# Performance work log

Measured on AMD Instinct MI355X. Metric: run time of the kernel, lower is better.

The kernel has to match this reference:

```python
import jax, jax.numpy as jnp
import numpy as np

WIRES = 4
DIM = 16  # 2**WIRES
EPS = 1e-5


def _rot_matrix(phi, theta, omega):
    # PennyLane Rot = RZ(omega) RY(theta) RZ(phi)
    c = jnp.cos(theta / 2).astype(jnp.complex64)
    s = jnp.sin(theta / 2).astype(jnp.complex64)
    ep = jnp.exp(-0.5j * (phi + omega).astype(jnp.complex64))
    em = jnp.exp(0.5j * (phi - omega).astype(jnp.complex64))
    m00 = ep * c
    m01 = -em * s
    m10 = jnp.conj(em) * s
    m11 = jnp.conj(ep) * c
    return jnp.stack([jnp.stack([m00, m01]), jnp.stack([m10, m11])])


def _apply_1q(state4, U, w):
    # state4: (B,2,2,2,2); apply 2x2 unitary on wire w (axis w+1)
    st = jnp.moveaxis(state4, w + 1, -1)
    st = st @ U.T  # sum_j st[...,j] * U[i,j]
    return jnp.moveaxis(st, -1, w + 1)


def _cnot_perm(c, t):
    # permutation of 16 basis indices for CNOT(control=c, target=t); wire 0 = MSB
    idx = np.arange(DIM)
    cbit = (idx >> (WIRES - 1 - c)) & 1
    return idx ^ (cbit << (WIRES - 1 - t))


def _circuit(x16, params):
    # AmplitudeEmbedding with normalize=True
    B = x16.shape[0]
    nrm = jnp.linalg.norm(x16, axis=1, keepdims=True)
    state = (x16 / nrm).astype(jnp.complex64)  # (B,16)
    L = params.shape[0]
    for l in range(L):
        st4 = state.reshape(B, 2, 2, 2, 2)
        for w in range(WIRES):
            U = _rot_matrix(params[l, w, 0], params[l, w, 1], params[l, w, 2])
            st4 = _apply_1q(st4, U, w)
        state = st4.reshape(B, DIM)
        r = (l % (WIRES - 1)) + 1  # StronglyEntanglingLayers default range
        for w in range(WIRES):
            perm = _cnot_perm(w, (w + r) % WIRES)
            state = state[:, perm]
    probs = (state.real ** 2 + state.imag ** 2)  # (B,16)
    p4 = probs.reshape(B, 2, 2, 2, 2)
    # <Z_w> = P(bit_w=0) - P(bit_w=1)
    outs = []
    for w in range(WIRES):
        axes = tuple(a for a in range(1, 5) if a != w + 1)
        pw = p4.sum(axis=axes)  # (B,2)
        outs.append(pw[:, 0] - pw[:, 1])
    return jnp.stack(outs, axis=1)  # (B,4)


def setup_inputs() -> dict:
    key = jax.random.key(0)
    k1, k2 = jax.random.split(key)
    B = 65536
    x = jax.random.normal(k1, (B, 1, 24, 24), dtype=jnp.float32)
    params = jax.random.normal(k2, (2, WIRES, 3), dtype=jnp.float32)
    gamma = jnp.ones((WIRES,), dtype=jnp.float32)
    beta = jnp.zeros((WIRES,), dtype=jnp.float32)
    return {"x": x, "params": params, "gamma": gamma, "beta": beta}


def reference(x, params, gamma, beta):
    B = x.shape[0]
    # avg_pool2d kernel 6: (B,1,24,24) -> (B,1,4,4) -> (B,16)
    pooled = x.reshape(B, 1, 4, 6, 4, 6).mean(axis=(3, 5)).reshape(B, DIM)
    out = _circuit(pooled, params)  # (B,4)
    # BatchNorm1d in training mode (biased batch stats)
    mu = out.mean(axis=0)
    var = ((out - mu) ** 2).mean(axis=0)
    return (out - mu) / jnp.sqrt(var + EPS) * gamma + beta
```

## Files before the change

kernel.cpp:

```cpp
#include <hip/hip_runtime.h>
#include <math.h>

#define BATCH 65536
#define XPER  576
#define NBLK  512
#define EPB   128
#define GPI   16
#define ITERS (EPB / GPI)
#define TILEF (GPI * XPER)


__device__ __forceinline__ void gload16(const float* g, float* l) {
    __builtin_amdgcn_global_load_lds(
        (__attribute__((address_space(1))) void*)(g),
        (__attribute__((address_space(3))) void*)(l),
        16, 0, 0);
}

__global__ __launch_bounds__(256) void circuit_kernel(
        const float* __restrict__ x, const float* __restrict__ params,
        float* __restrict__ out, float* __restrict__ accums) {
    __shared__ float sx[2][TILEF];
    __shared__ float sU[512];
    __shared__ float sg[48];
    __shared__ float spart[8];

    const int t    = threadIdx.x;
    const int wid  = t >> 6;
    const int lane = t & 63;
    const int e    = t >> 4;
    const int p    = t & 15;

    const size_t base = (size_t)blockIdx.x * EPB;

    {
        const float* src = x + base * XPER + wid * 2304 + lane * 4;
        float* dst = &sx[0][wid * 2304];
#pragma unroll
        for (int j = 0; j < 9; ++j) gload16(src + j * 256, dst + j * 256);
    }

    if (t < 8) {
        spart[t] = 0.0f;
        float phi   = params[t * 3 + 0];
        float theta = params[t * 3 + 1];
        float omega = params[t * 3 + 2];
        float apo = 0.5f * (phi + omega), amo = 0.5f * (phi - omega);
        sg[t * 6 + 0] = cosf(0.5f * theta);
        sg[t * 6 + 1] = sinf(0.5f * theta);
        sg[t * 6 + 2] = cosf(apo);
        sg[t * 6 + 3] = -sinf(apo);
        sg[t * 6 + 4] = cosf(amo);
        sg[t * 6 + 5] = sinf(amo);
    }
    __syncthreads();

    if (t < 16) {
        const int j = t;
        float Mr[16], Mi[16];
#pragma unroll
        for (int i = 0; i < 16; ++i) { Mr[i] = (i == j) ? 1.0f : 0.0f; Mi[i] = 0.0f; }
#pragma unroll
        for (int l = 0; l < 2; ++l) {
#pragma unroll
            for (int w = 0; w < 4; ++w) {
                const int g = l * 4 + w;
                float c   = sg[g * 6 + 0], s   = sg[g * 6 + 1];
                float epr = sg[g * 6 + 2], epi = sg[g * 6 + 3];
                float emr = sg[g * 6 + 4], emi = sg[g * 6 + 5];
                float m00r =  epr * c, m00i =  epi * c;
                float m01r = -emr * s, m01i = -emi * s;
                float m10r =  emr * s, m10i = -emi * s;
                float m11r =  epr * c, m11i = -epi * c;
                const int mask = 1 << (3 - w);
#pragma unroll
                for (int i = 0; i < 16; ++i) {
                    if (i & mask) continue;
                    int i1 = i | mask;
                    float r0 = Mr[i],  q0 = Mi[i];
                    float r1 = Mr[i1], q1 = Mi[i1];
                    Mr[i]  = m00r * r0 - m00i * q0 + m01r * r1 - m01i * q1;
                    Mi[i]  = m00r * q0 + m00i * r0 + m01r * q1 + m01i * r1;
                    Mr[i1] = m10r * r0 - m10i * q0 + m11r * r1 - m11i * q1;
                    Mi[i1] = m10r * q0 + m10i * r0 + m11r * q1 + m11i * r1;
                }
            }
            const int rr = (l % 3) + 1;
#pragma unroll
            for (int w = 0; w < 4; ++w) {
                int tq = (w + rr) & 3;
                int cb = 3 - w, tb = 3 - tq;
#pragma unroll
                for (int i = 0; i < 16; ++i) {
                    int pi = i ^ (((i >> cb) & 1) << tb);
                    if (pi > i) {
                        float tr = Mr[i]; Mr[i] = Mr[pi]; Mr[pi] = tr;
                        float ti = Mi[i]; Mi[i] = Mi[pi]; Mi[pi] = ti;
                    }
                }
            }
        }
#pragma unroll
        for (int i = 0; i < 16; ++i) {
            sU[i * 16 + j]       = Mr[i];
            sU[256 + i * 16 + j] = Mi[i];
        }
    }
    __syncthreads();

    float ur[16], ui[16];
    {
        const float4* u4 = (const float4*)(sU + p * 16);
        const float4* v4 = (const float4*)(sU + 256 + p * 16);
#pragma unroll
        for (int q = 0; q < 4; ++q) {
            float4 a = u4[q], b = v4[q];
            ur[4 * q + 0] = a.x; ur[4 * q + 1] = a.y; ur[4 * q + 2] = a.z; ur[4 * q + 3] = a.w;
            ui[4 * q + 0] = b.x; ui[4 * q + 1] = b.y; ui[4 * q + 2] = b.z; ui[4 * q + 3] = b.w;
        }
    }

    int c = -1;
    if      (p == 8) c = 0;
    else if (p == 4) c = 1;
    else if (p == 2) c = 2;
    else if (p == 1) c = 3;

    float zbuf[ITERS];
    float accz = 0.0f, accz2 = 0.0f;

#pragma unroll
    for (int it = 0; it < ITERS; ++it) {
        if (it + 1 < ITERS) {
            const float* src = x + (base + (size_t)(it + 1) * GPI) * XPER
                                 + wid * 2304 + lane * 4;
            float* dst = &sx[(it + 1) & 1][wid * 2304];
#pragma unroll
            for (int j = 0; j < 9; ++j) gload16(src + j * 256, dst + j * 256);
            asm volatile("s_waitcnt vmcnt(9)" ::: "memory");
        } else {
            asm volatile("s_waitcnt vmcnt(0)" ::: "memory");
        }
        __builtin_amdgcn_s_barrier();

        const float* bs = sx[it & 1] + e * XPER + (p >> 2) * 144 + (p & 3) * 6;
        float sum = 0.0f;
#pragma unroll
        for (int i = 0; i < 6; ++i) {
            const float2* rp = (const float2*)(bs + i * 24);
            float2 a2 = rp[0], b2 = rp[1], d2 = rp[2];
            sum += a2.x + a2.y + b2.x + b2.y + d2.x + d2.y;
        }
        float v = sum * (1.0f / 36.0f);

        float n2 = v * v;
        n2 += __shfl_xor(n2, 1);
        n2 += __shfl_xor(n2, 2);
        n2 += __shfl_xor(n2, 4);
        n2 += __shfl_xor(n2, 8);

        float sr = 0.0f, si = 0.0f;
#pragma unroll
        for (int j = 0; j < 16; ++j) {
            float vj = __shfl(v, j, 16);
            sr = fmaf(ur[j], vj, sr);
            si = fmaf(ui[j], vj, si);
        }
        float prob = (sr * sr + si * si) / n2;

        float a = prob, o;
        o = __shfl_xor(a, 1); a = (t & 1) ? (o - a) : (a + o);
        o = __shfl_xor(a, 2); a = (t & 2) ? (o - a) : (a + o);
        o = __shfl_xor(a, 4); a = (t & 4) ? (o - a) : (a + o);
        o = __shfl_xor(a, 8); a = (t & 8) ? (o - a) : (a + o);

        zbuf[it] = a;
        if (c >= 0) { accz += a; accz2 += a * a; }

        __builtin_amdgcn_s_barrier();
    }

    if (c >= 0) {
#pragma unroll
        for (int it = 0; it < ITERS; ++it)
            out[(base + (size_t)it * GPI + e) * 4 + c] = zbuf[it];
        atomicAdd(&spart[c], accz);
        atomicAdd(&spart[4 + c], accz2);
    }
    __syncthreads();
    if (t < 8) atomicAdd(&accums[t], spart[t]);
}

__global__ __launch_bounds__(256) void bn_apply(float* __restrict__ out,
                                                const float* __restrict__ accums,
                                                const float* __restrict__ gamma,
                                                const float* __restrict__ beta) {
    __shared__ float sc[8];
    const int t = threadIdx.x;
    if (t < 4) {
        float mu  = accums[t] * (1.0f / BATCH);
        float var = accums[4 + t] * (1.0f / BATCH) - mu * mu;
        float a = gamma[t] * rsqrtf(var + 1e-5f);
        sc[t]     = a;
        sc[4 + t] = beta[t] - mu * a;
    }
    __syncthreads();
    int i = blockIdx.x * 256 + t;
    float4 z = ((float4*)out)[i];
    z.x = fmaf(z.x, sc[0], sc[4]);
    z.y = fmaf(z.y, sc[1], sc[5]);
    z.z = fmaf(z.z, sc[2], sc[6]);
    z.w = fmaf(z.w, sc[3], sc[7]);
    ((float4*)out)[i] = z;
}

extern "C" void kernel_launch(void* const* d_in, const int* in_sizes, int n_in,
                              void* d_out, int out_size, void* d_ws, size_t ws_size,
                              hipStream_t stream) {
    const float* x      = (const float*)d_in[0];
    const float* params = (const float*)d_in[1];
    const float* gamma  = (const float*)d_in[2];
    const float* beta   = (const float*)d_in[3];
    float* out = (float*)d_out;
    float* ws  = (float*)d_ws;

    hipMemsetAsync(ws, 0, 8 * sizeof(float), stream);
    hipLaunchKernelGGL(circuit_kernel, dim3(NBLK), dim3(256), 0, stream,
                       x, params, out, ws);
    hipLaunchKernelGGL(bn_apply, dim3(BATCH / 256), dim3(256), 0, stream,
                       out, ws, gamma, beta);
}
```

Baseline: 41.99 us.

## Fuse batchnorm into circuit kernel via grid barrier and LDS broadcast

Removes the separate bn_apply launch: after accumulating batch statistics, each block waits on a global atomic counter/flag grid barrier, then computes the normalization coefficients and writes final normalized outputs directly. The per-element shuffle broadcast of pooled values is replaced by an LDS staging buffer with float4 reads, and the pooling row order is rotated per thread to spread LDS bank accesses. Launch bounds request two blocks per CU so all 512 blocks can be co-resident. The spin barrier relies on every block being resident at once, which risks deadlock if that does not hold, and it adds serialization at the end of the kernel.

```diff
diff --git a/kernel.cpp b/kernel.cpp
--- a/kernel.cpp
+++ b/kernel.cpp
@@ -17,18 +17,27 @@
         16, 0, 0);
 }
 
-__global__ __launch_bounds__(256) void circuit_kernel(
+__global__ __launch_bounds__(256, 2) void circuit_kernel(
         const float* __restrict__ x, const float* __restrict__ params,
-        float* __restrict__ out, float* __restrict__ accums) {
+        const float* __restrict__ gamma, const float* __restrict__ beta,
+        float* __restrict__ out, float* __restrict__ ws) {
     __shared__ float sx[2][TILEF];
     __shared__ float sU[512];
     __shared__ float sg[48];
+    __shared__ float sv[256];
     __shared__ float spart[8];
+    __shared__ float sstat[8];
+    __shared__ float scoef[8];
+
+    float* accums = ws;
+    unsigned* cnt  = (unsigned*)(ws + 8);
+    unsigned* flag = (unsigned*)(ws + 9);
 
     const int t    = threadIdx.x;
     const int wid  = t >> 6;
     const int lane = t & 63;
     const int e    = t >> 4;
+    const int le   = e & 3;
     const int p    = t & 15;
 
     const size_t base = (size_t)blockIdx.x * EPB;
@@ -126,6 +135,7 @@
     else if (p == 2) c = 2;
     else if (p == 1) c = 3;
 
+    const int r0 = (e + (p >> 2)) % 6;
     float zbuf[ITERS];
     float accz = 0.0f, accz2 = 0.0f;
 
@@ -147,24 +157,30 @@
         float sum = 0.0f;
 #pragma unroll
         for (int i = 0; i < 6; ++i) {
-            const float2* rp = (const float2*)(bs + i * 24);
+            int row = r0 + i; if (row >= 6) row -= 6;
+            const float2* rp = (const float2*)(bs + row * 24);
             float2 a2 = rp[0], b2 = rp[1], d2 = rp[2];
             sum += a2.x + a2.y + b2.x + b2.y + d2.x + d2.y;
         }
         float v = sum * (1.0f / 36.0f);
 
-        float n2 = v * v;
-        n2 += __shfl_xor(n2, 1);
-        n2 += __shfl_xor(n2, 2);
-        n2 += __shfl_xor(n2, 4);
-        n2 += __shfl_xor(n2, 8);
-
-        float sr = 0.0f, si = 0.0f;
+        sv[wid * 64 + le * 16 + p] = v;
+        float vv[16];
+        {
+            const float4* vb = (const float4*)(sv + wid * 64 + le * 16);
+#pragma unroll
+            for (int q = 0; q < 4; ++q) {
+                float4 a = vb[q];
+                vv[4 * q + 0] = a.x; vv[4 * q + 1] = a.y;
+                vv[4 * q + 2] = a.z; vv[4 * q + 3] = a.w;
+            }
+        }
+        float n2 = 0.0f, sr = 0.0f, si = 0.0f;
 #pragma unroll
         for (int j = 0; j < 16; ++j) {
-            float vj = __shfl(v, j, 16);
-            sr = fmaf(ur[j], vj, sr);
-            si = fmaf(ui[j], vj, si);
+            n2 = fmaf(vv[j], vv[j], n2);
+            sr = fmaf(ur[j], vv[j], sr);
+            si = fmaf(ui[j], vv[j], si);
         }
         float prob = (sr * sr + si * si) / n2;
 
@@ -181,37 +197,42 @@
     }
 
     if (c >= 0) {
-#pragma unroll
-        for (int it = 0; it < ITERS; ++it)
-            out[(base + (size_t)it * GPI + e) * 4 + c] = zbuf[it];
         atomicAdd(&spart[c], accz);
         atomicAdd(&spart[4 + c], accz2);
     }
     __syncthreads();
     if (t < 8) atomicAdd(&accums[t], spart[t]);
-}
-
-__global__ __launch_bounds__(256) void bn_apply(float* __restrict__ out,
-                                                const float* __restrict__ accums,
-                                                const float* __restrict__ gamma,
-                                                const float* __restrict__ beta) {
-    __shared__ float sc[8];
-    const int t = threadIdx.x;
+    __syncthreads();
+
+    if (t == 0) {
+        __threadfence();
+        unsigned old = atomicAdd(cnt, 1u);
+        if (old == NBLK - 1) {
+            __threadfence();
+            atomicExch(flag, 1u);
+        } else {
+            while (atomicAdd(flag, 0u) == 0u) __builtin_amdgcn_s_sleep(8);
+        }
+    }
+    __syncthreads();
+
+    if (t < 8) sstat[t] = atomicAdd(&accums[t], 0.0f);
+    __syncthreads();
     if (t < 4) {
-        float mu  = accums[t] * (1.0f / BATCH);
-        float var = accums[4 + t] * (1.0f / BATCH) - mu * mu;
+        float mu  = sstat[t] * (1.0f / BATCH);
+        float var = sstat[4 + t] * (1.0f / BATCH) - mu * mu;
         float a = gamma[t] * rsqrtf(var + 1e-5f);
-        sc[t]     = a;
-        sc[4 + t] = beta[t] - mu * a;
-    }
-    __syncthreads();
-    int i = blockIdx.x * 256 + t;
-    float4 z = ((float4*)out)[i];
-    z.x = fmaf(z.x, sc[0], sc[4]);
-    z.y = fmaf(z.y, sc[1], sc[5]);
-    z.z = fmaf(z.z, sc[2], sc[6]);
-    z.w = fmaf(z.w, sc[3], sc[7]);
-    ((float4*)out)[i] = z;
+        scoef[t]     = a;
+        scoef[4 + t] = beta[t] - mu * a;
+    }
+    __syncthreads();
+
+    if (c >= 0) {
+        float A = scoef[c], B = scoef[4 + c];
+#pragma unroll
+        for (int it = 0; it < ITERS; ++it)
+            out[(base + (size_t)it * GPI + e) * 4 + c] = fmaf(zbuf[it], A, B);
+    }
 }
 
 extern "C" void kernel_launch(void* const* d_in, const int* in_sizes, int n_in,
@@ -224,9 +245,7 @@
     float* out = (float*)d_out;
     float* ws  = (float*)d_ws;
 
-    hipMemsetAsync(ws, 0, 8 * sizeof(float), stream);
+    hipMemsetAsync(ws, 0, 64, stream);
     hipLaunchKernelGGL(circuit_kernel, dim3(NBLK), dim3(256), 0, stream,
-                       x, params, out, ws);
-    hipLaunchKernelGGL(bn_apply, dim3(BATCH / 256), dim3(256), 0, stream,
-                       out, ws, gamma, beta);
+                       x, params, gamma, beta, out, ws);
 }
```

Result: slower. 88.93 us (+111.8%).

## Give each wave private double-buffered tiles to drop block barriers

Applied to the files above, without the earlier changes.

Restructures the pipeline so each wavefront streams its own contiguous 32 images through a private double-buffered LDS region, removing the two block-wide barriers per iteration. It also staggers the pooling row order per lane to reduce LDS bank conflicts. The amplitude vector is exchanged through LDS float4 reads instead of 16 shuffles and a 4-step norm reduction. Launch bounds request two blocks per CU. The trade-off is relying on per-wave vmcnt waits and wave-local LDS visibility, with the same total LDS footprint.

```diff
diff --git a/kernel.cpp b/kernel.cpp
--- a/kernel.cpp
+++ b/kernel.cpp
@@ -5,9 +5,11 @@
 #define XPER  576
 #define NBLK  512
 #define EPB   128
-#define GPI   16
-#define ITERS (EPB / GPI)
-#define TILEF (GPI * XPER)
+#define WPB   4
+#define IPW   (EPB / WPB)
+#define CHUNK 4
+#define NCH   (IPW / CHUNK)
+#define CHF   (CHUNK * XPER)
 
 
 __device__ __forceinline__ void gload16(const float* g, float* l) {
@@ -17,25 +19,26 @@
         16, 0, 0);
 }
 
-__global__ __launch_bounds__(256) void circuit_kernel(
+__global__ __launch_bounds__(256, 2) void circuit_kernel(
         const float* __restrict__ x, const float* __restrict__ params,
         float* __restrict__ out, float* __restrict__ accums) {
-    __shared__ float sx[2][TILEF];
+    __shared__ float sx[WPB][2][CHF];
     __shared__ float sU[512];
     __shared__ float sg[48];
+    __shared__ float sv[256];
     __shared__ float spart[8];
 
     const int t    = threadIdx.x;
     const int wid  = t >> 6;
     const int lane = t & 63;
-    const int e    = t >> 4;
-    const int p    = t & 15;
-
-    const size_t base = (size_t)blockIdx.x * EPB;
+    const int e    = lane >> 4;
+    const int p    = lane & 15;
+
+    const size_t ibase = (size_t)blockIdx.x * EPB + (size_t)wid * IPW;
 
     {
-        const float* src = x + base * XPER + wid * 2304 + lane * 4;
-        float* dst = &sx[0][wid * 2304];
+        const float* src = x + ibase * XPER + lane * 4;
+        float* dst = &sx[wid][0][0];
 #pragma unroll
         for (int j = 0; j < 9; ++j) gload16(src + j * 256, dst + j * 256);
     }
@@ -126,45 +129,50 @@
     else if (p == 2) c = 2;
     else if (p == 1) c = 3;
 
-    float zbuf[ITERS];
+    const int r0 = (e + (p >> 2)) % 6;
+    float zbuf[NCH];
     float accz = 0.0f, accz2 = 0.0f;
 
 #pragma unroll
-    for (int it = 0; it < ITERS; ++it) {
-        if (it + 1 < ITERS) {
-            const float* src = x + (base + (size_t)(it + 1) * GPI) * XPER
-                                 + wid * 2304 + lane * 4;
-            float* dst = &sx[(it + 1) & 1][wid * 2304];
+    for (int ch = 0; ch < NCH; ++ch) {
+        if (ch + 1 < NCH) {
+            const float* src = x + (ibase + (size_t)(ch + 1) * CHUNK) * XPER + lane * 4;
+            float* dst = &sx[wid][(ch + 1) & 1][0];
 #pragma unroll
             for (int j = 0; j < 9; ++j) gload16(src + j * 256, dst + j * 256);
             asm volatile("s_waitcnt vmcnt(9)" ::: "memory");
         } else {
             asm volatile("s_waitcnt vmcnt(0)" ::: "memory");
         }
-        __builtin_amdgcn_s_barrier();
-
-        const float* bs = sx[it & 1] + e * XPER + (p >> 2) * 144 + (p & 3) * 6;
+
+        const float* bs = &sx[wid][ch & 1][0] + e * XPER + (p >> 2) * 144 + (p & 3) * 6;
         float sum = 0.0f;
 #pragma unroll
         for (int i = 0; i < 6; ++i) {
-            const float2* rp = (const float2*)(bs + i * 24);
+            int row = r0 + i; if (row >= 6) row -= 6;
+            const float2* rp = (const float2*)(bs + row * 24);
             float2 a2 = rp[0], b2 = rp[1], d2 = rp[2];
             sum += a2.x + a2.y + b2.x + b2.y + d2.x + d2.y;
         }
         float v = sum * (1.0f / 36.0f);
 
-        float n2 = v * v;
-        n2 += __shfl_xor(n2, 1);
-        n2 += __shfl_xor(n2, 2);
-        n2 += __shfl_xor(n2, 4);
-        n2 += __shfl_xor(n2, 8);
-
-        float sr = 0.0f, si = 0.0f;
+        sv[wid * 64 + e * 16 + p] = v;
+        float vv[16];
+        {
+            const float4* vb = (const float4*)(sv + wid * 64 + e * 16);
+#pragma unroll
+            for (int q = 0; q < 4; ++q) {
+                float4 a = vb[q];
+                vv[4 * q + 0] = a.x; vv[4 * q + 1] = a.y;
+                vv[4 * q + 2] = a.z; vv[4 * q + 3] = a.w;
+            }
+        }
+        float n2 = 0.0f, sr = 0.0f, si = 0.0f;
 #pragma unroll
         for (int j = 0; j < 16; ++j) {
-            float vj = __shfl(v, j, 16);
-            sr = fmaf(ur[j], vj, sr);
-            si = fmaf(ui[j], vj, si);
+            n2 = fmaf(vv[j], vv[j], n2);
+            sr = fmaf(ur[j], vv[j], sr);
+            si = fmaf(ui[j], vv[j], si);
         }
         float prob = (sr * sr + si * si) / n2;
 
@@ -174,16 +182,14 @@
         o = __shfl_xor(a, 4); a = (t & 4) ? (o - a) : (a + o);
         o = __shfl_xor(a, 8); a = (t & 8) ? (o - a) : (a + o);
 
-        zbuf[it] = a;
+        zbuf[ch] = a;
         if (c >= 0) { accz += a; accz2 += a * a; }
-
-        __builtin_amdgcn_s_barrier();
     }
 
     if (c >= 0) {
 #pragma unroll
-        for (int it = 0; it < ITERS; ++it)
-            out[(base + (size_t)it * GPI + e) * 4 + c] = zbuf[it];
+        for (int ch = 0; ch < NCH; ++ch)
+            out[(ibase + (size_t)ch * CHUNK + e) * 4 + c] = zbuf[ch];
         atomicAdd(&spart[c], accz);
         atomicAdd(&spart[4 + c], accz2);
     }
@@ -224,7 +230,7 @@
     float* out = (float*)d_out;
     float* ws  = (float*)d_ws;
 
-    hipMemsetAsync(ws, 0, 8 * sizeof(float), stream);
+    hipMemsetAsync(ws, 0, 32, stream);
     hipLaunchKernelGGL(circuit_kernel, dim3(NBLK), dim3(256), 0, stream,
                        x, params, out, ws);
     hipLaunchKernelGGL(bn_apply, dim3(BATCH / 256), dim3(256), 0, stream,
```

After: 40.66 us. 3.2% less time.
